# Performance work log

Measured on AMD Instinct MI355X. Metric: run time of the kernel, lower is better.

Reference implementation:

```python
import jax, jax.numpy as jnp
import numpy as np

BASE_SCALE = 60.0
EPS = 1e-8


def _nearest_D8(x):
    """Nearest point in D8 lattice (integer vectors with even coordinate sum), x: [..., 8]."""
    f = jnp.round(x)
    d = x - f
    parity_even = (jnp.mod(jnp.sum(f, axis=-1), 2.0) == 0.0)
    # flip rounding at the coordinate with the largest rounding error
    idx = jnp.argmax(jnp.abs(d), axis=-1)
    delta = jnp.where(d >= 0, 1.0, -1.0).astype(x.dtype)
    onehot = jax.nn.one_hot(idx, 8, dtype=x.dtype)
    flip = jnp.take_along_axis(delta, idx[..., None], axis=-1)
    g = f + onehot * flip
    return jnp.where(parity_even[..., None], f, g)


def _e8_quantize(x):
    """Nearest point in E8 = D8 U (D8 + 1/2), x: [..., 8]."""
    y0 = _nearest_D8(x)
    y1 = _nearest_D8(x - 0.5) + 0.5
    d0 = jnp.sum((x - y0) ** 2, axis=-1, keepdims=True)
    d1 = jnp.sum((x - y1) ** 2, axis=-1, keepdims=True)
    return jnp.where(d0 <= d1, y0, y1)


def _quantize_with_row_scaling(w):
    """Row-norm scale -> E8 lattice quantize on 8-dim blocks -> rescale back."""
    n_rows = w.shape[0]
    adaptive = min(2.0, max(0.5, n_rows / 10000.0))
    sf = jnp.asarray(BASE_SCALE * adaptive, dtype=w.dtype)
    row_norms = jnp.linalg.norm(w, axis=1, keepdims=True)  # [out, 1]
    row_norms_safe = jnp.maximum(row_norms, EPS)
    w_scaled = (w / row_norms_safe) * sf
    q = _e8_quantize(w_scaled.reshape(-1, 8)).reshape(w.shape)
    return q * row_norms_safe / sf


def setup_inputs() -> dict:
    key = jax.random.key(0)
    k1, k2, k3 = jax.random.split(key, 3)
    B, IN, OUT = 4096, 4096, 4096
    x = jax.random.normal(k1, (B, IN), dtype=jnp.float32)
    weight = jax.random.normal(k2, (OUT, IN), dtype=jnp.float32) * 0.1
    bias = jax.random.normal(k3, (OUT,), dtype=jnp.float32)
    return {"x": x, "weight": weight, "bias": bias}


def reference(x, weight, bias):
    wq = _quantize_with_row_scaling(weight)
    return x @ wq.T + bias
```

## Files before the change

kernel.cpp:

```cpp
#include <hip/hip_runtime.h>
#include <hip/hip_bf16.h>

typedef __bf16 bf16_t;
typedef __bf16 bf16x8 __attribute__((ext_vector_type(8)));
typedef float f32x4 __attribute__((ext_vector_type(4)));

#define GLL16(gp, lp)                                                          \
    __builtin_amdgcn_global_load_lds(                                          \
        (const __attribute__((address_space(1))) void*)(gp),                   \
        (__attribute__((address_space(3))) void*)(lp), 16, 0, 0)

#define SBAR() __builtin_amdgcn_s_barrier()
#define WAIT_VM4() asm volatile("s_waitcnt vmcnt(4)" ::: "memory")
#define WAIT_VM0() asm volatile("s_waitcnt vmcnt(0)" ::: "memory")
#define PH_SYNC()                                                              \
    do {                                                                       \
        __builtin_amdgcn_s_barrier();                                          \
        asm volatile("s_waitcnt lgkmcnt(0)" ::: "memory");                     \
        __builtin_amdgcn_sched_barrier(0);                                     \
    } while (0)
#define PH_END()                                                               \
    do {                                                                       \
        __builtin_amdgcn_s_setprio(0);                                         \
        __builtin_amdgcn_s_barrier();                                          \
    } while (0)
#define MFMA_(d, a, b)                                                         \
    d = __builtin_amdgcn_mfma_f32_16x16x32_bf16(a, b, d, 0, 0, 0)


__device__ __forceinline__ void nearest_D8_d(const double x[8], double f[8]) {
    double d[8];
    double fs = 0.0;
#pragma unroll
    for (int i = 0; i < 8; ++i) {
        f[i] = rint(x[i]);
        d[i] = x[i] - f[i];
        fs += f[i];
    }
    long long s = (long long)fs;
    if (s & 1LL) {
        int idx = 0;
        double best = fabs(d[0]);
#pragma unroll
        for (int i = 1; i < 8; ++i) {
            double a = fabs(d[i]);
            if (a > best) { best = a; idx = i; }
        }
        f[idx] += (d[idx] >= 0.0) ? 1.0 : -1.0;
    }
}

__device__ __forceinline__ void e8_quantize_d(const double x[8], float q[8]) {
    double y0[8], y1[8], xs[8];
    nearest_D8_d(x, y0);
#pragma unroll
    for (int i = 0; i < 8; ++i) xs[i] = x[i] - 0.5;
    nearest_D8_d(xs, y1);
#pragma unroll
    for (int i = 0; i < 8; ++i) y1[i] += 0.5;
    double d0 = 0.0, d1 = 0.0;
#pragma unroll
    for (int i = 0; i < 8; ++i) {
        double a = x[i] - y0[i]; d0 += a * a;
        double b = x[i] - y1[i]; d1 += b * b;
    }
    bool take0 = (d0 <= d1);
#pragma unroll
    for (int i = 0; i < 8; ++i) q[i] = (float)(take0 ? y0[i] : y1[i]);
}

__global__ __launch_bounds__(256) void quant_kernel(
    const float* __restrict__ W, bf16_t* __restrict__ Q,
    float* __restrict__ scale, int IN, double sfd)
{
    const int row  = blockIdx.x;
    const int t    = threadIdx.x;
    const int lane = t & 63, w = t >> 6;
    const float* wrow = W + (size_t)row * IN;

    double ss = 0.0;
    for (int i = t; i < (IN >> 2); i += 256) {
        float4 v = *(const float4*)(wrow + i * 4);
        double a = v.x, b = v.y, c = v.z, d = v.w;
        ss += a * a + b * b + c * c + d * d;
    }
#pragma unroll
    for (int m = 1; m < 64; m <<= 1) ss += __shfl_xor(ss, m);
    __shared__ double red[4];
    if (lane == 0) red[w] = ss;
    __syncthreads();
    double S   = (red[0] + red[1]) + (red[2] + red[3]);
    double nsd = fmax(sqrt(S), 1e-8);

    for (int b = t; b < (IN >> 3); b += 256) {
        const float* xp = wrow + b * 8;
        float4 v0 = *(const float4*)xp;
        float4 v1 = *(const float4*)(xp + 4);
        double xd[8] = {v0.x, v0.y, v0.z, v0.w, v1.x, v1.y, v1.z, v1.w};
        double xsd[8];
#pragma unroll
        for (int i = 0; i < 8; ++i) xsd[i] = (xd[i] / nsd) * sfd;
        float qf[8];
        e8_quantize_d(xsd, qf);
        bf16x8 o;
#pragma unroll
        for (int i = 0; i < 8; ++i) o[i] = (bf16_t)qf[i];
        *(bf16x8*)(Q + (size_t)row * IN + b * 8) = o;
    }
    if (t == 0) scale[row] = (float)(nsd / sfd);
}


__global__ void cvt_kernel(const float* __restrict__ x, bf16_t* __restrict__ y,
                           long long n8)
{
    long long i = (long long)blockIdx.x * blockDim.x + threadIdx.x;
    long long stride = (long long)gridDim.x * blockDim.x;
    for (; i < n8; i += stride) {
        float4 v0 = *(const float4*)(x + i * 8);
        float4 v1 = *(const float4*)(x + i * 8 + 4);
        bf16x8 o;
        o[0] = (bf16_t)v0.x; o[1] = (bf16_t)v0.y;
        o[2] = (bf16_t)v0.z; o[3] = (bf16_t)v0.w;
        o[4] = (bf16_t)v1.x; o[5] = (bf16_t)v1.y;
        o[6] = (bf16_t)v1.z; o[7] = (bf16_t)v1.w;
        *(bf16x8*)(y + i * 8) = o;
    }
}


#define BM 256
#define BN 256
#define BK 64

__global__ __launch_bounds__(512, 2) void gemm_kernel(
    const bf16_t* __restrict__ A,
    const bf16_t* __restrict__ B,
    const float* __restrict__ scale,
    const float* __restrict__ bias,
    float* __restrict__ C,
    int M, int N, int K)
{
    __shared__ __align__(16) bf16_t lds[2][2][2][8192];

    const int t    = threadIdx.x;
    const int lane = t & 63;
    const int w    = t >> 6;
    const int wr   = w >> 2;
    const int wc   = w & 3;

    const int nwg = gridDim.x;
    const int bid = blockIdx.x;
    const int q8 = nwg >> 3, r8 = nwg & 7;
    const int xcd = bid & 7, idx = bid >> 3;
    const int swz = (xcd < r8 ? xcd * (q8 + 1) : r8 * (q8 + 1) + (xcd - r8) * q8) + idx;
    const int nbx = N / BN;
    const int bx = swz % nbx, by = swz / nbx;

    const int rowq  = t >> 3;
    const int kslot = ((t & 7) ^ (rowq & 7)) << 3;
    const bf16_t* gA = A + (size_t)(by * BM + rowq) * K + kslot;
    const bf16_t* gB = B + (size_t)(bx * BN + rowq) * K + kslot;

#define STAGE(isB, bufi, h, kt)                                                \
    do {                                                                       \
        const bf16_t* s_ = ((isB) ? gB : gA)                                   \
            + (size_t)(h) * 128 * (size_t)K + (size_t)(kt) * BK;               \
        GLL16(s_,                   &lds[bufi][isB][h][t * 8]);                \
        GLL16(s_ + 64 * (size_t)K,  &lds[bufi][isB][h][t * 8 + 4096]);         \
    } while (0)

    const int l15  = lane & 15;
    const int koff = lane >> 4;
    const int aoff0 = l15 * 64 + (((koff)     ^ (lane & 7)) << 3);
    const int aoff1 = l15 * 64 + (((4 + koff) ^ (lane & 7)) << 3);

    f32x4 acc[8][4];
    const f32x4 zero = {0.f, 0.f, 0.f, 0.f};
#pragma unroll
    for (int R = 0; R < 8; ++R)
#pragma unroll
        for (int Cf = 0; Cf < 4; ++Cf) acc[R][Cf] = zero;

    const int NT = K / BK;

    STAGE(0, 0, 0, 0); STAGE(0, 0, 1, 0);
    STAGE(1, 0, 0, 0); STAGE(1, 0, 1, 0);
    STAGE(0, 1, 0, 1); STAGE(0, 1, 1, 1);
    WAIT_VM4();
    SBAR();

    bf16x8 af[4][2], b01[2][2], b23[2][2];

    for (int kt = 0; kt < NT; ++kt) {
        const int cur = kt & 1;
        const bf16_t* ldsA = &lds[cur][0][wr][0];
        const bf16_t* ldsB = &lds[cur][1][wc >> 1][(wc & 1) * 4096];
        const bool sb = (kt + 1 < NT);
        const bool sa = (kt + 2 < NT);

#pragma unroll
        for (int R = 0; R < 4; ++R) {
            af[R][0] = *(const bf16x8*)(ldsA + R * 1024 + aoff0);
            af[R][1] = *(const bf16x8*)(ldsA + R * 1024 + aoff1);
        }
#pragma unroll
        for (int c = 0; c < 2; ++c) {
            b01[c][0] = *(const bf16x8*)(ldsB + c * 1024 + aoff0);
            b01[c][1] = *(const bf16x8*)(ldsB + c * 1024 + aoff1);
        }
        if (sb) STAGE(1, cur ^ 1, 0, kt + 1);
        PH_SYNC();
        __builtin_amdgcn_s_setprio(1);
#pragma unroll
        for (int R = 0; R < 4; ++R)
#pragma unroll
            for (int s = 0; s < 2; ++s) {
                MFMA_(acc[R][0], af[R][s], b01[0][s]);
                MFMA_(acc[R][1], af[R][s], b01[1][s]);
            }
        PH_END();

#pragma unroll
        for (int c = 0; c < 2; ++c) {
            b23[c][0] = *(const bf16x8*)(ldsB + (2 + c) * 1024 + aoff0);
            b23[c][1] = *(const bf16x8*)(ldsB + (2 + c) * 1024 + aoff1);
        }
        if (sb) STAGE(1, cur ^ 1, 1, kt + 1);
        PH_SYNC();
        __builtin_amdgcn_s_setprio(1);
#pragma unroll
        for (int R = 0; R < 4; ++R)
#pragma unroll
            for (int s = 0; s < 2; ++s) {
                MFMA_(acc[R][2], af[R][s], b23[0][s]);
                MFMA_(acc[R][3], af[R][s], b23[1][s]);
            }
        PH_END();

#pragma unroll
        for (int R = 0; R < 4; ++R) {
            af[R][0] = *(const bf16x8*)(ldsA + (4 + R) * 1024 + aoff0);
            af[R][1] = *(const bf16x8*)(ldsA + (4 + R) * 1024 + aoff1);
        }
        PH_SYNC();
        __builtin_amdgcn_s_setprio(1);
#pragma unroll
        for (int R = 0; R < 4; ++R)
#pragma unroll
            for (int s = 0; s < 2; ++s) {
                MFMA_(acc[4 + R][2], af[R][s], b23[0][s]);
                MFMA_(acc[4 + R][3], af[R][s], b23[1][s]);
            }
        PH_END();

#pragma unroll
        for (int c = 0; c < 2; ++c) {
            b01[c][0] = *(const bf16x8*)(ldsB + c * 1024 + aoff0);
            b01[c][1] = *(const bf16x8*)(ldsB + c * 1024 + aoff1);
        }
        if (sa) { STAGE(0, cur, 0, kt + 2); STAGE(0, cur, 1, kt + 2); }
        if (kt < NT - 2) { WAIT_VM4(); }
        else if (kt == NT - 2) { WAIT_VM0(); }
        PH_SYNC();
        __builtin_amdgcn_s_setprio(1);
#pragma unroll
        for (int R = 0; R < 4; ++R)
#pragma unroll
            for (int s = 0; s < 2; ++s) {
                MFMA_(acc[4 + R][0], af[R][s], b01[0][s]);
                MFMA_(acc[4 + R][1], af[R][s], b01[1][s]);
            }
        PH_END();
    }

    const int r0 = by * BM + wr * 128 + (lane >> 4) * 4;
    const int c0 = bx * BN + wc * 64 + l15;
#pragma unroll
    for (int Cf = 0; Cf < 4; ++Cf) {
        const int col = c0 + Cf * 16;
        const float sc = scale[col];
        const float bi = bias[col];
#pragma unroll
        for (int R = 0; R < 8; ++R) {
            const int row = r0 + R * 16;
#pragma unroll
            for (int j = 0; j < 4; ++j)
                C[(size_t)(row + j) * N + col] = acc[R][Cf][j] * sc + bi;
        }
    }
#undef STAGE
}


extern "C" void kernel_launch(void* const* d_in, const int* in_sizes, int n_in,
                              void* d_out, int out_size, void* d_ws, size_t ws_size,
                              hipStream_t stream)
{
    const float* x    = (const float*)d_in[0];
    const float* wgt  = (const float*)d_in[1];
    const float* bias = (const float*)d_in[2];

    const int OUT = in_sizes[2];
    const int IN  = (int)((long long)in_sizes[1] / OUT);
    const int M   = (int)((long long)in_sizes[0] / IN);
    const int N = OUT, K = IN;

    double ad = (double)OUT / 10000.0;
    if (ad < 0.5) ad = 0.5;
    if (ad > 2.0) ad = 2.0;
    const double sfd = 60.0 * ad;

    bf16_t* Q  = (bf16_t*)d_ws;
    bf16_t* Xb = (bf16_t*)((char*)d_ws + (size_t)OUT * IN * sizeof(bf16_t));
    float*  sc = (float*)((char*)d_ws + (size_t)OUT * IN * sizeof(bf16_t)
                                      + (size_t)M * IN * sizeof(bf16_t));
    float*  C  = (float*)d_out;

    quant_kernel<<<OUT, 256, 0, stream>>>(wgt, Q, sc, IN, sfd);

    long long n8 = (long long)M * IN / 8;
    int cblocks = (int)((n8 + 255) / 256);
    if (cblocks > 2048) cblocks = 2048;
    cvt_kernel<<<cblocks, 256, 0, stream>>>(x, Xb, n8);

    int grid = (M / BM) * (N / BN);
    gemm_kernel<<<grid, 512, 0, stream>>>(Xb, Q, sc, bias, C, M, N, K);
}
```

Measured before the change: 177.9 us.

## Merge quant and convert kernels; prefetch both GEMM operands two stages ahead

The weight quantization and activation bf16 conversion now run in one launch, with block ranges split between the two jobs. This removes a kernel boundary and lets the two memory-bound passes overlap. In the GEMM main loop, both A and B tiles are now staged two iterations ahead into the buffer just consumed, with a relaxed vmcnt wait. The redundant b01 reload is dropped and the MFMA loop order is swapped to interleave k-steps. Risks include LDS reuse hazards from overwriting the current buffer mid-iteration, and changed wait counts.

New measurement: 171.1 us. 3.8% less time.

```diff
diff --git a/kernel.cpp b/kernel.cpp
--- a/kernel.cpp
+++ b/kernel.cpp
@@ -11,7 +11,7 @@
         (__attribute__((address_space(3))) void*)(lp), 16, 0, 0)
 
 #define SBAR() __builtin_amdgcn_s_barrier()
-#define WAIT_VM4() asm volatile("s_waitcnt vmcnt(4)" ::: "memory")
+#define WAIT_VM8() asm volatile("s_waitcnt vmcnt(8)" ::: "memory")
 #define WAIT_VM0() asm volatile("s_waitcnt vmcnt(0)" ::: "memory")
 #define PH_SYNC()                                                              \
     do {                                                                       \
@@ -69,10 +69,27 @@
     for (int i = 0; i < 8; ++i) q[i] = (float)(take0 ? y0[i] : y1[i]);
 }
 
-__global__ __launch_bounds__(256) void quant_kernel(
+__global__ __launch_bounds__(256) void prep_kernel(
     const float* __restrict__ W, bf16_t* __restrict__ Q,
-    float* __restrict__ scale, int IN, double sfd)
+    float* __restrict__ scale, int IN, double sfd,
+    const float* __restrict__ x, bf16_t* __restrict__ Xb, long long n8,
+    int OUT, int CB)
 {
+    if (blockIdx.x >= (unsigned)OUT) {
+        long long i = (long long)(blockIdx.x - OUT) * 256 + threadIdx.x;
+        long long stride = (long long)CB * 256;
+        for (; i < n8; i += stride) {
+            float4 v0 = *(const float4*)(x + i * 8);
+            float4 v1 = *(const float4*)(x + i * 8 + 4);
+            bf16x8 o;
+            o[0] = (bf16_t)v0.x; o[1] = (bf16_t)v0.y;
+            o[2] = (bf16_t)v0.z; o[3] = (bf16_t)v0.w;
+            o[4] = (bf16_t)v1.x; o[5] = (bf16_t)v1.y;
+            o[6] = (bf16_t)v1.z; o[7] = (bf16_t)v1.w;
+            *(bf16x8*)(Xb + i * 8) = o;
+        }
+        return;
+    }
     const int row  = blockIdx.x;
     const int t    = threadIdx.x;
     const int lane = t & 63, w = t >> 6;
@@ -108,24 +125,6 @@
         *(bf16x8*)(Q + (size_t)row * IN + b * 8) = o;
     }
     if (t == 0) scale[row] = (float)(nsd / sfd);
-}
-
-
-__global__ void cvt_kernel(const float* __restrict__ x, bf16_t* __restrict__ y,
-                           long long n8)
-{
-    long long i = (long long)blockIdx.x * blockDim.x + threadIdx.x;
-    long long stride = (long long)gridDim.x * blockDim.x;
-    for (; i < n8; i += stride) {
-        float4 v0 = *(const float4*)(x + i * 8);
-        float4 v1 = *(const float4*)(x + i * 8 + 4);
-        bf16x8 o;
-        o[0] = (bf16_t)v0.x; o[1] = (bf16_t)v0.y;
-        o[2] = (bf16_t)v0.z; o[3] = (bf16_t)v0.w;
-        o[4] = (bf16_t)v1.x; o[5] = (bf16_t)v1.y;
-        o[6] = (bf16_t)v1.z; o[7] = (bf16_t)v1.w;
-        *(bf16x8*)(y + i * 8) = o;
-    }
 }
 
 
@@ -184,10 +183,15 @@
 
     const int NT = K / BK;
 
+    STAGE(1, 0, 0, 0); STAGE(1, 0, 1, 0);
     STAGE(0, 0, 0, 0); STAGE(0, 0, 1, 0);
-    STAGE(1, 0, 0, 0); STAGE(1, 0, 1, 0);
-    STAGE(0, 1, 0, 1); STAGE(0, 1, 1, 1);
-    WAIT_VM4();
+    if (NT > 1) {
+        STAGE(1, 1, 0, 1); STAGE(1, 1, 1, 1);
+        STAGE(0, 1, 0, 1); STAGE(0, 1, 1, 1);
+        WAIT_VM8();
+    } else {
+        WAIT_VM0();
+    }
     SBAR();
 
     bf16x8 af[4][2], b01[2][2], b23[2][2];
@@ -196,8 +200,7 @@
         const int cur = kt & 1;
         const bf16_t* ldsA = &lds[cur][0][wr][0];
         const bf16_t* ldsB = &lds[cur][1][wc >> 1][(wc & 1) * 4096];
-        const bool sb = (kt + 1 < NT);
-        const bool sa = (kt + 2 < NT);
+        const bool s2 = (kt + 2 < NT);
 
 #pragma unroll
         for (int R = 0; R < 4; ++R) {
@@ -209,13 +212,13 @@
             b01[c][0] = *(const bf16x8*)(ldsB + c * 1024 + aoff0);
             b01[c][1] = *(const bf16x8*)(ldsB + c * 1024 + aoff1);
         }
-        if (sb) STAGE(1, cur ^ 1, 0, kt + 1);
+        asm volatile("s_waitcnt lgkmcnt(8)" ::: "memory");
         PH_SYNC();
         __builtin_amdgcn_s_setprio(1);
 #pragma unroll
-        for (int R = 0; R < 4; ++R)
-#pragma unroll
-            for (int s = 0; s < 2; ++s) {
+        for (int s = 0; s < 2; ++s)
+#pragma unroll
+            for (int R = 0; R < 4; ++R) {
                 MFMA_(acc[R][0], af[R][s], b01[0][s]);
                 MFMA_(acc[R][1], af[R][s], b01[1][s]);
             }
@@ -226,13 +229,12 @@
             b23[c][0] = *(const bf16x8*)(ldsB + (2 + c) * 1024 + aoff0);
             b23[c][1] = *(const bf16x8*)(ldsB + (2 + c) * 1024 + aoff1);
         }
-        if (sb) STAGE(1, cur ^ 1, 1, kt + 1);
         PH_SYNC();
         __builtin_amdgcn_s_setprio(1);
 #pragma unroll
-        for (int R = 0; R < 4; ++R)
-#pragma unroll
-            for (int s = 0; s < 2; ++s) {
+        for (int s = 0; s < 2; ++s)
+#pragma unroll
+            for (int R = 0; R < 4; ++R) {
                 MFMA_(acc[R][2], af[R][s], b23[0][s]);
                 MFMA_(acc[R][3], af[R][s], b23[1][s]);
             }
@@ -243,34 +245,30 @@
             af[R][0] = *(const bf16x8*)(ldsA + (4 + R) * 1024 + aoff0);
             af[R][1] = *(const bf16x8*)(ldsA + (4 + R) * 1024 + aoff1);
         }
+        if (s2) { STAGE(1, cur, 0, kt + 2); STAGE(1, cur, 1, kt + 2); }
         PH_SYNC();
         __builtin_amdgcn_s_setprio(1);
 #pragma unroll
-        for (int R = 0; R < 4; ++R)
-#pragma unroll
-            for (int s = 0; s < 2; ++s) {
+        for (int s = 0; s < 2; ++s)
+#pragma unroll
+            for (int R = 0; R < 4; ++R) {
                 MFMA_(acc[4 + R][2], af[R][s], b23[0][s]);
                 MFMA_(acc[4 + R][3], af[R][s], b23[1][s]);
             }
         PH_END();
 
-#pragma unroll
-        for (int c = 0; c < 2; ++c) {
-            b01[c][0] = *(const bf16x8*)(ldsB + c * 1024 + aoff0);
-            b01[c][1] = *(const bf16x8*)(ldsB + c * 1024 + aoff1);
-        }
-        if (sa) { STAGE(0, cur, 0, kt + 2); STAGE(0, cur, 1, kt + 2); }
-        if (kt < NT - 2) { WAIT_VM4(); }
-        else if (kt == NT - 2) { WAIT_VM0(); }
+        if (s2) { STAGE(0, cur, 0, kt + 2); STAGE(0, cur, 1, kt + 2); }
         PH_SYNC();
         __builtin_amdgcn_s_setprio(1);
 #pragma unroll
-        for (int R = 0; R < 4; ++R)
-#pragma unroll
-            for (int s = 0; s < 2; ++s) {
+        for (int s = 0; s < 2; ++s)
+#pragma unroll
+            for (int R = 0; R < 4; ++R) {
                 MFMA_(acc[4 + R][0], af[R][s], b01[0][s]);
                 MFMA_(acc[4 + R][1], af[R][s], b01[1][s]);
             }
+        if (kt < NT - 2) { WAIT_VM8(); }
+        else if (kt == NT - 2) { WAIT_VM0(); }
         PH_END();
     }
 
@@ -317,12 +315,10 @@
                                       + (size_t)M * IN * sizeof(bf16_t));
     float*  C  = (float*)d_out;
 
-    quant_kernel<<<OUT, 256, 0, stream>>>(wgt, Q, sc, IN, sfd);
-
     long long n8 = (long long)M * IN / 8;
-    int cblocks = (int)((n8 + 255) / 256);
-    if (cblocks > 2048) cblocks = 2048;
-    cvt_kernel<<<cblocks, 256, 0, stream>>>(x, Xb, n8);
+    const int CB = 2048;
+    prep_kernel<<<OUT + CB, 256, 0, stream>>>(wgt, Q, sc, IN, sfd,
+                                              x, Xb, n8, OUT, CB);
 
     int grid = (M / BM) * (N / BN);
     gemm_kernel<<<grid, 512, 0, stream>>>(Xb, Q, sc, bias, C, M, N, K);
```
